# Kernel tuning notes

Hardware: AMD Instinct MI355X
Metric: run time of the kernel (lower is better)

## Reference

```python
import jax, jax.numpy as jnp
import numpy as np

H, W = 56, 56
N = H * W
C = 2
THETA_ALPHA = 160.0
THETA_BETA = 3.0
THETA_GAMMA = 3.0
NUM_ITERATIONS = 10


def setup_inputs() -> dict:
    key = jax.random.key(0)
    k1, k2, k3, k4 = jax.random.split(key, 4)
    inputs = jax.random.uniform(k1, (2, H, W), dtype=jnp.float32)
    # Keras 'uniform' initializer: U(-0.05, 0.05)
    sp_w = jax.random.uniform(k2, (C, C), minval=-0.05, maxval=0.05, dtype=jnp.float32)
    bl_w = jax.random.uniform(k3, (C, C), minval=-0.05, maxval=0.05, dtype=jnp.float32)
    compat = jax.random.uniform(k4, (C, C), minval=-0.05, maxval=0.05, dtype=jnp.float32)
    return {"inputs": inputs, "spatial_ker_weights": sp_w,
            "bilateral_ker_weights": bl_w, "compatibility_matrix": compat}


def _sqdist(f):
    # f: [N, D] -> [N, N] squared pairwise distances
    s = jnp.sum(f * f, axis=1)
    return s[:, None] + s[None, :] - 2.0 * (f @ f.T)


def _kernels(rgb_flat):
    # rgb_flat: [N, 3] pixel colors (0..255)
    ys, xs = jnp.meshgrid(jnp.arange(H, dtype=jnp.float32),
                          jnp.arange(W, dtype=jnp.float32), indexing="ij")
    pos = jnp.stack([xs.reshape(-1), ys.reshape(-1)], axis=1)  # [N, 2]
    # spatial (Gaussian) kernel: exp(-||p-q||^2 / (2*gamma^2))
    k_sp = jnp.exp(-0.5 * _sqdist(pos / THETA_GAMMA))
    # bilateral kernel: positions scaled by alpha, colors by beta
    f_bl = jnp.concatenate([pos / THETA_ALPHA, rgb_flat / THETA_BETA], axis=1)
    k_bl = jnp.exp(-0.5 * _sqdist(f_bl))
    return k_sp, k_bl


def reference(inputs, spatial_ker_weights, bilateral_ker_weights, compatibility_matrix):
    unary = inputs[0]            # [H, W], foreground prob
    gray = inputs[1] * 255.0     # [H, W], image intensities scaled as in the layer

    # unaries: [C, H, W] with channel 0 = 1-u, channel 1 = u
    unaries = jnp.stack([1.0 - unary, unary], axis=0).reshape(C, N)

    rgb_flat = jnp.tile(gray.reshape(-1)[:, None], (1, 3))  # [N, 3]

    k_sp, k_bl = _kernels(rgb_flat)
    ones = jnp.ones((N,), dtype=jnp.float32)
    norm_sp = k_sp @ ones  # [N]
    norm_bl = k_bl @ ones  # [N]

    q = unaries
    for i in range(NUM_ITERATIONS):
        softmax_out = q if i == 0 else jax.nn.softmax(q, axis=0)
        spatial_out = (softmax_out @ k_sp) / norm_sp[None, :]     # [C, N]
        bilateral_out = (softmax_out @ k_bl) / norm_bl[None, :]   # [C, N]
        message = spatial_ker_weights @ spatial_out + bilateral_ker_weights @ bilateral_out
        pairwise = compatibility_matrix @ message                 # [C, N]
        q = unaries - pairwise

    cur_q = q.reshape(C, H, W).transpose(1, 2, 0)  # [H, W, C]
    obj_prob = jax.nn.softmax(cur_q, axis=2)[:, :, 1]
    return obj_prob.reshape(1, H, W)
```

## Files before the change

kernel.cpp:

```cpp
#include <hip/hip_runtime.h>


namespace {

constexpr int NPIX = 3136;
constexpr int WIMG = 56;
constexpr int JPB  = 16;
constexpr int NBLK = NPIX / JPB;
constexpr int NTHR = 512;
constexpr int NQ   = NPIX / 4;
constexpr int NBUF = 9;
constexpr int Q2   = NQ - NTHR;
constexpr int NBIN = 128;
constexpr int BANDB = 5;
constexpr int NCHK = 98;
constexpr int CPX  = 32;
constexpr int UTRIP = 10;

constexpr float LOG2E = 1.4426950408889634f;
constexpr float C1 = -LOG2E / 18.0f;
constexpr float C2 = -LOG2E / 51200.0f;
constexpr float C3 = -LOG2E / 6.0f;

constexpr int O_SSH  = 0;
constexpr int O_SSRT = 12544;
constexpr int O_GXY  = 25088;
constexpr int O_MSRT = 50176;
constexpr int O_RANK = 56448;
constexpr int O_OFF  = 62720;
constexpr int O_WSX  = 63248;
constexpr int O_WSY  = 66832;
constexpr int O_LIDX = 70416;
constexpr int O_WBND = 73552;
constexpr int POOLSZ = 94032;

#define REDUCE32(v) \
    { v += __shfl_xor(v, 1); v += __shfl_xor(v, 2); v += __shfl_xor(v, 4); \
      v += __shfl_xor(v, 8); v += __shfl_xor(v, 16); }
#define REDUCE64(v) \
    { v += __shfl_xor(v, 1); v += __shfl_xor(v, 2); v += __shfl_xor(v, 4); \
      v += __shfl_xor(v, 8); v += __shfl_xor(v, 16); v += __shfl_xor(v, 32); }

__global__ __launch_bounds__(NTHR) void crf_all(
    const float* __restrict__ inp,
    const float* __restrict__ spw, const float* __restrict__ blw,
    const float* __restrict__ cmw,
    float* sbufs, float* __restrict__ out)
{
    __shared__ __align__(16) unsigned char pool[POOLSZ];
    float*  s_sh  = (float*)(pool + O_SSH);
    float4* s_sh4 = (float4*)(pool + O_SSH);
    float*  s_srt = (float*)(pool + O_SSRT);
    float2* gxy   = (float2*)(pool + O_GXY);
    unsigned short* m_srt = (unsigned short*)(pool + O_MSRT);
    unsigned short* rank  = (unsigned short*)(pool + O_RANK);
    unsigned*       offs  = (unsigned*)(pool + O_OFF);
    float*  wsx   = (float*)(pool + O_WSX);
    float*  wsy   = (float*)(pool + O_WSY);
    unsigned char*  lidx = (unsigned char*)(pool + O_LIDX);
    float*  wband = (float*)(pool + O_WBND);
    unsigned short* H  = (unsigned short*)(pool + O_SSH);
    unsigned*       Hz = (unsigned*)(pool + O_SSH);

    const int t   = threadIdx.x;
    const int bid = blockIdx.x;
    const int sub = t & 31;
    const int jl  = t >> 5;
    const int j   = bid * JPB + jl;
    const int xj  = j % WIMG;
    const int yj  = j / WIMG;
    const float xjf = (float)xj, yjf = (float)yj;

    const float uj = inp[j];
    const float gj = inp[NPIX + j] * 255.0f;

    const float e0 = cmw[2] - cmw[0];
    const float e1 = cmw[3] - cmw[1];
    const float alpha = e0 * (spw[0] + blw[0]) + e1 * (spw[2] + blw[2]);
    const float beta  = e0 * (spw[1] - spw[0]) + e1 * (spw[3] - spw[2]);
    const float gamma = e0 * (blw[1] - blw[0]) + e1 * (blw[3] - blw[2]);

    for (int i = t; i < 6272; i += NTHR) Hz[i] = 0u;
    for (int idx = t; idx < JPB * 56; idx += NTHR) {
        const int jlw = idx / 56, p = idx - jlw * 56;
        const int jj = bid * JPB + jlw;
        const float ddx = (float)(jj % WIMG - p);
        const float ddy = (float)(jj / WIMG - p);
        wsx[idx] = __builtin_amdgcn_exp2f(C1 * ddx * ddx);
        wsy[idx] = __builtin_amdgcn_exp2f(C1 * ddy * ddy);
    }
    __syncthreads();
    if (t < NCHK) {
        unsigned short* Hr = H + t * NBIN;
        const int mb = t * CPX;
        for (int i = 0; i < CPX; ++i) {
            int b = (int)(inp[NPIX + mb + i] * 255.0f);
            b = (b > 255 ? 255 : b) >> 1;
            lidx[mb + i] = (unsigned char)Hr[b];
            Hr[b] = (unsigned short)(Hr[b] + 1);
        }
    }
    __syncthreads();
    if (t < NBIN) {
        unsigned run = 0;
        for (int c = 0; c < NCHK; ++c) {
            unsigned short v = H[c * NBIN + t];
            H[c * NBIN + t] = (unsigned short)run;
            run += v;
        }
        offs[t] = run;
    }
    __syncthreads();
    if (t < 64) {
        unsigned v0 = offs[2 * t], v1 = offs[2 * t + 1];
        unsigned sum = v0 + v1;
        unsigned sc = sum;
        for (int d = 1; d < 64; d <<= 1) {
            unsigned n = __shfl_up(sc, d);
            if (t >= d) sc += n;
        }
        unsigned base = sc - sum;
        offs[2 * t] = base;
        offs[2 * t + 1] = base + v0;
        if (t == 63) offs[NBIN] = sc;
    }
    __syncthreads();
    for (int m = t; m < NPIX; m += NTHR) {
        int b = (int)(inp[NPIX + m] * 255.0f);
        b = (b > 255 ? 255 : b) >> 1;
        const int r = (int)offs[b] + (int)H[(m >> 5) * NBIN + b] + (int)lidx[m];
        m_srt[r] = (unsigned short)m;
        rank[m]  = (unsigned short)r;
    }
    __syncthreads();
    for (int p = t; p < NPIX; p += NTHR) {
        const int m = (int)m_srt[p];
        s_srt[p] = inp[m];
        const int yi = (m * 9363) >> 19;
        const int xi = m - yi * 56;
        gxy[p] = make_float2(inp[NPIX + m] * 255.0f, (float)(xi + 64 * yi));
    }
    {
        const float4* u4 = (const float4*)inp;
        for (int q = t; q < NQ; q += NTHR) s_sh4[q] = u4[q];
    }
    __syncthreads();

    float sx, sy;
    {
        float dd = xjf - (float)sub;
        sx = __builtin_amdgcn_exp2f(C1 * dd * dd);
        if (sub + 32 < 56) {
            float d2 = xjf - (float)(sub + 32);
            sx += __builtin_amdgcn_exp2f(C1 * d2 * d2);
        }
        REDUCE32(sx);
        dd = yjf - (float)sub;
        sy = __builtin_amdgcn_exp2f(C1 * dd * dd);
        if (sub + 32 < 56) {
            float d2 = yjf - (float)(sub + 32);
            sy += __builtin_amdgcn_exp2f(C1 * d2 * d2);
        }
        REDUCE32(sy);
    }
    const float rnsp = 1.0f / (sx * sy);

    int bj = (int)gj; bj = (bj > 255 ? 255 : bj) >> 1;
    const int b0 = bj < BANDB ? 0 : bj - BANDB;
    const int b1 = bj + BANDB > NBIN - 1 ? NBIN - 1 : bj + BANDB;
    const int blo = (int)offs[b0];
    const int bhi = (int)offs[b1 + 1];

    auto spatial = [&]() -> float {
        const int wv = t >> 6;
        const int ln = t & 63;
        float v0 = 0.f, v1 = 0.f;
        if (ln < 56) {
            const float4* S = s_sh4 + ln * 14;
            float4 sv[14];
#pragma unroll
            for (int q = 0; q < 14; ++q) sv[q] = S[q];
            const int c0 = wv * 2, c1 = c0 + 1;
            const float4* R0 = (const float4*)(wsx + c0 * 56);
            const float4* R1 = (const float4*)(wsx + c1 * 56);
            float a0 = 0.f, a1 = 0.f;
#pragma unroll
            for (int q = 0; q < 14; ++q) {
                float4 w0 = R0[q], w1 = R1[q];
                a0 = fmaf(w0.x, sv[q].x, a0); a0 = fmaf(w0.y, sv[q].y, a0);
                a0 = fmaf(w0.z, sv[q].z, a0); a0 = fmaf(w0.w, sv[q].w, a0);
                a1 = fmaf(w1.x, sv[q].x, a1); a1 = fmaf(w1.y, sv[q].y, a1);
                a1 = fmaf(w1.z, sv[q].z, a1); a1 = fmaf(w1.w, sv[q].w, a1);
            }
            v0 = wsy[c0 * 56 + ln] * a0;
            v1 = wsy[c1 * 56 + ln] * a1;
        }
        REDUCE64(v0); REDUCE64(v1);
        return (ln < 32) ? v0 : v1;
    };

    auto bilateral0 = [&](float* nacc_out) -> float {
        float acc = 0.f, nacc = 0.f;
        const int pb = blo + sub;
        float* wb = wband + jl * (UTRIP * 32);
#pragma unroll
        for (int i = 0; i < UTRIP; ++i) {
            const int pp = pb + i * 32;
            const int pc = pp < bhi ? pp : bhi - 1;
            const float2 gx = gxy[pc];
            const float sv  = s_srt[pc];
            const float yi  = floorf(gx.y * 0.015625f);
            const float xi  = fmaf(-64.f, yi, gx.y);
            const float ux = xi - xjf, vy = yi - yjf;
            const float r2 = fmaf(ux, ux, vy * vy);
            const float dg = gx.x - gj;
            float w = __builtin_amdgcn_exp2f(fmaf(dg * C3, dg, r2 * C2));
            w = (pp < bhi) ? w : 0.0f;
            wb[i * 32 + sub] = w;
            acc = fmaf(w, sv, acc);
            nacc += w;
        }
        for (int pp = pb + UTRIP * 32; pp < bhi; pp += 32) {
            const float2 gx = gxy[pp];
            const float sv  = s_srt[pp];
            const float yi  = floorf(gx.y * 0.015625f);
            const float xi  = fmaf(-64.f, yi, gx.y);
            const float ux = xi - xjf, vy = yi - yjf;
            const float r2 = fmaf(ux, ux, vy * vy);
            const float dg = gx.x - gj;
            const float w = __builtin_amdgcn_exp2f(fmaf(dg * C3, dg, r2 * C2));
            acc = fmaf(w, sv, acc);
            nacc += w;
        }
        REDUCE32(acc); REDUCE32(nacc);
        *nacc_out = nacc;
        return acc;
    };

    auto bilateralK = [&]() -> float {
        float acc = 0.f;
        const int pb = blo + sub;
        const float* wb = wband + jl * (UTRIP * 32);
#pragma unroll
        for (int i = 0; i < UTRIP; ++i) {
            const int pp = pb + i * 32;
            const int pc = pp < bhi ? pp : bhi - 1;
            const float w  = wb[i * 32 + sub];
            const float sv = s_srt[pc];
            acc = fmaf(w, sv, acc);
        }
        for (int pp = pb + UTRIP * 32; pp < bhi; pp += 32) {
            const float2 gx = gxy[pp];
            const float sv  = s_srt[pp];
            const float yi  = floorf(gx.y * 0.015625f);
            const float xi  = fmaf(-64.f, yi, gx.y);
            const float ux = xi - xjf, vy = yi - yjf;
            const float r2 = fmaf(ux, ux, vy * vy);
            const float dg = gx.x - gj;
            const float w = __builtin_amdgcn_exp2f(fmaf(dg * C3, dg, r2 * C2));
            acc = fmaf(w, sv, acc);
        }
        REDUCE32(acc);
        return acc;
    };

    auto publish_sync = [&](float s, float* buf) {
        if (sub == 0)
            __hip_atomic_store(&buf[j], s, __ATOMIC_RELAXED,
                               __HIP_MEMORY_SCOPE_AGENT);
        const float4* src = (const float4*)buf;
        float4 a, b;
        const bool two = (t < Q2);
        bool da = false, db = !two;
        for (;;) {
            if (!da)
                asm volatile("global_load_dwordx4 %0, %1, off sc0 sc1"
                             : "=&v"(a) : "v"(src + t));
            if (!db)
                asm volatile("global_load_dwordx4 %0, %1, off sc0 sc1"
                             : "=&v"(b) : "v"(src + NTHR + t));
            asm volatile("s_waitcnt vmcnt(0)" ::: "memory");
            if (!da) da = (fminf(fminf(a.x, a.y), fminf(a.z, a.w)) != 0.0f);
            if (!db) db = (fminf(fminf(b.x, b.y), fminf(b.z, b.w)) != 0.0f);
            if (da && db) break;
        }
        s_sh4[t] = a;
        {
            const int p4 = 4 * t;
            s_srt[rank[p4 + 0]] = a.x;
            s_srt[rank[p4 + 1]] = a.y;
            s_srt[rank[p4 + 2]] = a.z;
            s_srt[rank[p4 + 3]] = a.w;
        }
        if (two) {
            s_sh4[NTHR + t] = b;
            const int p4 = 4 * (NTHR + t);
            s_srt[rank[p4 + 0]] = b.x;
            s_srt[rank[p4 + 1]] = b.y;
            s_srt[rank[p4 + 2]] = b.z;
            s_srt[rank[p4 + 3]] = b.w;
        }
        __syncthreads();
    };

    const float base = 2.0f * uj - 1.0f - alpha;
    float rnbl, s;

    {
        float tsp = spatial();
        float nacc;
        float acc = bilateral0(&nacc);
        rnbl = 1.0f / nacc;
        float d = base - beta * (tsp * rnsp) - gamma * (acc * rnbl);
        s = 1.0f / (1.0f + __builtin_amdgcn_exp2f(-d * LOG2E));
    }
    publish_sync(s, sbufs);

    for (int k = 1; k < 10; ++k) {
        float tsp = spatial();
        float acc = bilateralK();
        float d = base - beta * (tsp * rnsp) - gamma * (acc * rnbl);
        s = 1.0f / (1.0f + __builtin_amdgcn_exp2f(-d * LOG2E));
        if (k < 9) publish_sync(s, sbufs + k * NPIX);
        else if (sub == 0) out[j] = s;
    }
}

}

extern "C" void kernel_launch(void* const* d_in, const int* in_sizes, int n_in,
                              void* d_out, int out_size, void* d_ws, size_t ws_size,
                              hipStream_t stream) {
    const float* inp = (const float*)d_in[0];
    const float* spw = (const float*)d_in[1];
    const float* blw = (const float*)d_in[2];
    const float* cmw = (const float*)d_in[3];
    float* sbufs = (float*)d_ws;
    float* out = (float*)d_out;

    hipMemsetAsync(sbufs, 0, NBUF * NPIX * sizeof(float), stream);
    crf_all<<<dim3(NBLK), dim3(NTHR), 0, stream>>>(inp, spw, blw, cmw,
                                                   sbufs, out);
}
```

Measured before the change: 59.52 us.

## Drop sorted state copy; gather via index and cache band weights in registers

Removes the color-sorted copy of the softmax state (s_srt) and the rank scatter that rebuilt it after every iteration. The bilateral loops now gather state through the sorted pixel index m_srt. The band weights and indices are kept in per-thread registers instead of an LDS buffer. The spatial reduction is also restructured to do one combined 32-lane reduce instead of two 64-lane reduces. This shrinks LDS use and removes scatter work from each sync step, at the cost of indirect LDS gathers with possible bank conflicts and more registers.

```diff
diff --git a/kernel.cpp b/kernel.cpp
--- a/kernel.cpp
+++ b/kernel.cpp
@@ -23,23 +23,17 @@
 constexpr float C3 = -LOG2E / 6.0f;
 
 constexpr int O_SSH  = 0;
-constexpr int O_SSRT = 12544;
-constexpr int O_GXY  = 25088;
-constexpr int O_MSRT = 50176;
-constexpr int O_RANK = 56448;
-constexpr int O_OFF  = 62720;
-constexpr int O_WSX  = 63248;
-constexpr int O_WSY  = 66832;
-constexpr int O_LIDX = 70416;
-constexpr int O_WBND = 73552;
-constexpr int POOLSZ = 94032;
+constexpr int O_GXY  = 12544;
+constexpr int O_MSRT = 37632;
+constexpr int O_OFF  = 43904;
+constexpr int O_WSX  = 44432;
+constexpr int O_WSY  = 48016;
+constexpr int O_LIDX = 51600;
+constexpr int POOLSZ = 54736;
 
 #define REDUCE32(v) \
     { v += __shfl_xor(v, 1); v += __shfl_xor(v, 2); v += __shfl_xor(v, 4); \
       v += __shfl_xor(v, 8); v += __shfl_xor(v, 16); }
-#define REDUCE64(v) \
-    { v += __shfl_xor(v, 1); v += __shfl_xor(v, 2); v += __shfl_xor(v, 4); \
-      v += __shfl_xor(v, 8); v += __shfl_xor(v, 16); v += __shfl_xor(v, 32); }
 
 __global__ __launch_bounds__(NTHR) void crf_all(
     const float* __restrict__ inp,
@@ -50,15 +44,12 @@
     __shared__ __align__(16) unsigned char pool[POOLSZ];
     float*  s_sh  = (float*)(pool + O_SSH);
     float4* s_sh4 = (float4*)(pool + O_SSH);
-    float*  s_srt = (float*)(pool + O_SSRT);
     float2* gxy   = (float2*)(pool + O_GXY);
     unsigned short* m_srt = (unsigned short*)(pool + O_MSRT);
-    unsigned short* rank  = (unsigned short*)(pool + O_RANK);
     unsigned*       offs  = (unsigned*)(pool + O_OFF);
     float*  wsx   = (float*)(pool + O_WSX);
     float*  wsy   = (float*)(pool + O_WSY);
     unsigned char*  lidx = (unsigned char*)(pool + O_LIDX);
-    float*  wband = (float*)(pool + O_WBND);
     unsigned short* H  = (unsigned short*)(pool + O_SSH);
     unsigned*       Hz = (unsigned*)(pool + O_SSH);
 
@@ -130,12 +121,10 @@
         b = (b > 255 ? 255 : b) >> 1;
         const int r = (int)offs[b] + (int)H[(m >> 5) * NBIN + b] + (int)lidx[m];
         m_srt[r] = (unsigned short)m;
-        rank[m]  = (unsigned short)r;
     }
     __syncthreads();
     for (int p = t; p < NPIX; p += NTHR) {
         const int m = (int)m_srt[p];
-        s_srt[p] = inp[m];
         const int yi = (m * 9363) >> 19;
         const int xi = m - yi * 56;
         gxy[p] = make_float2(inp[NPIX + m] * 255.0f, (float)(xi + 64 * yi));
@@ -195,20 +184,26 @@
             v0 = wsy[c0 * 56 + ln] * a0;
             v1 = wsy[c1 * 56 + ln] * a1;
         }
-        REDUCE64(v0); REDUCE64(v1);
-        return (ln < 32) ? v0 : v1;
+        v0 += __shfl_xor(v0, 32);
+        v1 += __shfl_xor(v1, 32);
+        float z = (ln < 32) ? v0 : v1;
+        z += __shfl_xor(z, 1); z += __shfl_xor(z, 2); z += __shfl_xor(z, 4);
+        z += __shfl_xor(z, 8); z += __shfl_xor(z, 16);
+        return z;
     };
+
+    int   m_reg[UTRIP];
+    float w_reg[UTRIP];
 
     auto bilateral0 = [&](float* nacc_out) -> float {
         float acc = 0.f, nacc = 0.f;
         const int pb = blo + sub;
-        float* wb = wband + jl * (UTRIP * 32);
 #pragma unroll
         for (int i = 0; i < UTRIP; ++i) {
             const int pp = pb + i * 32;
             const int pc = pp < bhi ? pp : bhi - 1;
             const float2 gx = gxy[pc];
-            const float sv  = s_srt[pc];
+            const int   m  = (int)m_srt[pc];
             const float yi  = floorf(gx.y * 0.015625f);
             const float xi  = fmaf(-64.f, yi, gx.y);
             const float ux = xi - xjf, vy = yi - yjf;
@@ -216,13 +211,14 @@
             const float dg = gx.x - gj;
             float w = __builtin_amdgcn_exp2f(fmaf(dg * C3, dg, r2 * C2));
             w = (pp < bhi) ? w : 0.0f;
-            wb[i * 32 + sub] = w;
-            acc = fmaf(w, sv, acc);
+            m_reg[i] = m;
+            w_reg[i] = w;
+            acc = fmaf(w, s_sh[m], acc);
             nacc += w;
         }
         for (int pp = pb + UTRIP * 32; pp < bhi; pp += 32) {
             const float2 gx = gxy[pp];
-            const float sv  = s_srt[pp];
+            const float sv  = s_sh[(int)m_srt[pp]];
             const float yi  = floorf(gx.y * 0.015625f);
             const float xi  = fmaf(-64.f, yi, gx.y);
             const float ux = xi - xjf, vy = yi - yjf;
@@ -239,19 +235,13 @@
 
     auto bilateralK = [&]() -> float {
         float acc = 0.f;
+#pragma unroll
+        for (int i = 0; i < UTRIP; ++i)
+            acc = fmaf(w_reg[i], s_sh[m_reg[i]], acc);
         const int pb = blo + sub;
-        const float* wb = wband + jl * (UTRIP * 32);
-#pragma unroll
-        for (int i = 0; i < UTRIP; ++i) {
-            const int pp = pb + i * 32;
-            const int pc = pp < bhi ? pp : bhi - 1;
-            const float w  = wb[i * 32 + sub];
-            const float sv = s_srt[pc];
-            acc = fmaf(w, sv, acc);
-        }
         for (int pp = pb + UTRIP * 32; pp < bhi; pp += 32) {
             const float2 gx = gxy[pp];
-            const float sv  = s_srt[pp];
+            const float sv  = s_sh[(int)m_srt[pp]];
             const float yi  = floorf(gx.y * 0.015625f);
             const float xi  = fmaf(-64.f, yi, gx.y);
             const float ux = xi - xjf, vy = yi - yjf;
@@ -285,21 +275,7 @@
             if (da && db) break;
         }
         s_sh4[t] = a;
-        {
-            const int p4 = 4 * t;
-            s_srt[rank[p4 + 0]] = a.x;
-            s_srt[rank[p4 + 1]] = a.y;
-            s_srt[rank[p4 + 2]] = a.z;
-            s_srt[rank[p4 + 3]] = a.w;
-        }
-        if (two) {
-            s_sh4[NTHR + t] = b;
-            const int p4 = 4 * (NTHR + t);
-            s_srt[rank[p4 + 0]] = b.x;
-            s_srt[rank[p4 + 1]] = b.y;
-            s_srt[rank[p4 + 2]] = b.z;
-            s_srt[rank[p4 + 3]] = b.w;
-        }
+        if (two) s_sh4[NTHR + t] = b;
         __syncthreads();
     };
 
```

New measurement: 64.41 us. 1.08x slower.
